# Performance work log

Measured on AMD Instinct MI355X. Metric: run time of the kernel, lower is better.

## Reference

```python
import jax, jax.numpy as jnp
import numpy as np

DENSE_SIZE = 2048
BATCH = 64
MAX_SPIKES = 1024


def setup_inputs() -> dict:
    key = jax.random.key(0)
    k_w, k_ids, k_ns = jax.random.split(key, 3)
    # weights ~ N(0, 2) as in tf.random_normal_initializer(0., 2., 42)
    W = jax.random.normal(k_w, (DENSE_SIZE, DENSE_SIZE), dtype=jnp.float32) * 2.0
    spike_ids = jax.random.randint(k_ids, (BATCH, MAX_SPIKES), 0, DENSE_SIZE, dtype=jnp.int32)
    num_spikes = jax.random.randint(k_ns, (BATCH,), 0, MAX_SPIKES, dtype=jnp.int32)
    return {"spike_ids": spike_ids, "num_spikes": num_spikes, "W": W}


def reference(spike_ids, num_spikes, W):
    # Dense-weight x binary-sparse-vector matmul:
    # out[b, j] = sum_{i < num_spikes[b]} W[j, spike_ids[b, i]]
    # i.e. gather active columns of W and sum them.
    mask = (jnp.arange(MAX_SPIKES)[None, :] < num_spikes[:, None]).astype(W.dtype)  # [B, S]
    cols = jnp.take(W.T, spike_ids, axis=0)  # [B, S, D] gathered columns (rows of W.T)
    out = jnp.einsum('bs,bsd->bd', mask, cols)  # [B, D]
    return out
```

## Files before the change

kernel.cpp:

```cpp
#include <hip/hip_runtime.h>

#define DENSE 2048
#define BATCH 64
#define MAXS  1024

typedef __attribute__((ext_vector_type(8))) __bf16 bf16x8;
typedef __attribute__((ext_vector_type(4))) float f32x4;


__global__ __launch_bounds__(256) void hist_kernel(const int* __restrict__ ids,
                                                   const int* __restrict__ ns,
                                                   __bf16* __restrict__ Cbf,
                                                   float* __restrict__ out) {
    __shared__ int cnt[DENSE];
    const int b = blockIdx.x;
    const int tid = threadIdx.x;
    #pragma unroll
    for (int k = tid; k < DENSE; k += 256) cnt[k] = 0;
    __syncthreads();
    const int n = ns[b];
    const int4 v = ((const int4*)(ids + b * MAXS))[tid];
    const int base = tid * 4;
    if (base + 0 < n) atomicAdd(&cnt[v.x], 1);
    if (base + 1 < n) atomicAdd(&cnt[v.y], 1);
    if (base + 2 < n) atomicAdd(&cnt[v.z], 1);
    if (base + 3 < n) atomicAdd(&cnt[v.w], 1);
    __syncthreads();
    const int mt = b >> 4;
    const int bl = b & 15;
    #pragma unroll
    for (int k = tid; k < DENSE; k += 256) {
        const int lane = bl | (((k >> 3) & 3) << 4);
        const size_t off = (size_t)(((k >> 5) * 4 + mt) * 64 + lane) * 8 + (k & 7);
        Cbf[off] = (__bf16)(float)cnt[k];
        out[(size_t)b * DENSE + k] = 0.0f;
    }
}

__global__ __launch_bounds__(256) void spmm_kernel(const float* __restrict__ W,
                                                   const __bf16* __restrict__ Cbf,
                                                   float* __restrict__ out) {
    const int tid  = threadIdx.x;
    const int lane = tid & 63;
    const int wv   = tid >> 6;
    const int j0   = blockIdx.x * 16;
    const int ks4  = blockIdx.y;

    const int ln = lane & 15;
    const int lq = lane >> 4;

    const int step0 = ks4 * 16 + wv * 4;
    const float* wrow = W + (size_t)(j0 + ln) * DENSE;

    f32x4 w0[4], w1[4];
    #pragma unroll
    for (int s = 0; s < 4; ++s) {
        const int kbase = (step0 + s) * 32 + lq * 8;
        w0[s] = *(const f32x4*)(wrow + kbase);
        w1[s] = *(const f32x4*)(wrow + kbase + 4);
    }
    bf16x8 afr[4][4];
    #pragma unroll
    for (int s = 0; s < 4; ++s) {
        #pragma unroll
        for (int mt = 0; mt < 4; ++mt) {
            afr[s][mt] = *(const bf16x8*)(Cbf + ((size_t)((step0 + s) * 4 + mt) * 64 + lane) * 8);
        }
    }

    bf16x8 wb[4];
    #pragma unroll
    for (int s = 0; s < 4; ++s) {
        #pragma unroll
        for (int i = 0; i < 4; ++i) {
            wb[s][i]     = (__bf16)w0[s][i];
            wb[s][i + 4] = (__bf16)w1[s][i];
        }
    }

    f32x4 acc[4];
    #pragma unroll
    for (int mt = 0; mt < 4; ++mt) acc[mt] = (f32x4)0.0f;
    #pragma unroll
    for (int s = 0; s < 4; ++s) {
        #pragma unroll
        for (int mt = 0; mt < 4; ++mt) {
            acc[mt] = __builtin_amdgcn_mfma_f32_16x16x32_bf16(afr[s][mt], wb[s], acc[mt], 0, 0, 0);
        }
    }

    __shared__ float P[4][4][4][64];
    #pragma unroll
    for (int mt = 0; mt < 4; ++mt) {
        #pragma unroll
        for (int r = 0; r < 4; ++r) {
            P[wv][mt][r][lane] = acc[mt][r];
        }
    }
    __syncthreads();

    const int jloc  = tid & 15;
    const int bpart = tid >> 4;
    const int lsrc  = ((bpart >> 2) << 4) | jloc;
    const int r     = bpart & 3;
    #pragma unroll
    for (int mt = 0; mt < 4; ++mt) {
        const float v = P[0][mt][r][lsrc] + P[1][mt][r][lsrc]
                      + P[2][mt][r][lsrc] + P[3][mt][r][lsrc];
        atomicAdd(&out[(size_t)(mt * 16 + bpart) * DENSE + j0 + jloc], v);
    }
}

extern "C" void kernel_launch(void* const* d_in, const int* in_sizes, int n_in,
                              void* d_out, int out_size, void* d_ws, size_t ws_size,
                              hipStream_t stream) {
    const int*   ids = (const int*)d_in[0];
    const int*   ns  = (const int*)d_in[1];
    const float* W   = (const float*)d_in[2];
    float*  out = (float*)d_out;
    __bf16* Cbf = (__bf16*)d_ws;

    hipLaunchKernelGGL(hist_kernel, dim3(BATCH), dim3(256), 0, stream, ids, ns, Cbf, out);
    hipLaunchKernelGGL(spmm_kernel, dim3(128, 4), dim3(256), 0, stream, W, Cbf, out);
}
```

Measured before the change: 71.39 us.

## Fuse histogram and SpMM into one cooperative kernel with grid sync

Merges the histogram and MFMA SpMM kernels into one cooperative launch of 512 blocks. The first 64 blocks build the per-batch count matrix and zero the output, and every block prefetches and converts its W tile before a grid-wide barrier. After the barrier the blocks read the counts and run the MFMA accumulation. This removes the second kernel launch and overlaps the W loads with the histogram work, at the cost of a grid sync and a cooperative launch that needs all blocks resident at once.

```diff
diff --git a/kernel.cpp b/kernel.cpp
--- a/kernel.cpp
+++ b/kernel.cpp
@@ -1,54 +1,32 @@
 #include <hip/hip_runtime.h>
+#include <hip/hip_cooperative_groups.h>
 
 #define DENSE 2048
 #define BATCH 64
 #define MAXS  1024
 
+namespace cg = cooperative_groups;
+
 typedef __attribute__((ext_vector_type(8))) __bf16 bf16x8;
 typedef __attribute__((ext_vector_type(4))) float f32x4;
 
 
-__global__ __launch_bounds__(256) void hist_kernel(const int* __restrict__ ids,
-                                                   const int* __restrict__ ns,
-                                                   __bf16* __restrict__ Cbf,
-                                                   float* __restrict__ out) {
-    __shared__ int cnt[DENSE];
-    const int b = blockIdx.x;
-    const int tid = threadIdx.x;
-    #pragma unroll
-    for (int k = tid; k < DENSE; k += 256) cnt[k] = 0;
-    __syncthreads();
-    const int n = ns[b];
-    const int4 v = ((const int4*)(ids + b * MAXS))[tid];
-    const int base = tid * 4;
-    if (base + 0 < n) atomicAdd(&cnt[v.x], 1);
-    if (base + 1 < n) atomicAdd(&cnt[v.y], 1);
-    if (base + 2 < n) atomicAdd(&cnt[v.z], 1);
-    if (base + 3 < n) atomicAdd(&cnt[v.w], 1);
-    __syncthreads();
-    const int mt = b >> 4;
-    const int bl = b & 15;
-    #pragma unroll
-    for (int k = tid; k < DENSE; k += 256) {
-        const int lane = bl | (((k >> 3) & 3) << 4);
-        const size_t off = (size_t)(((k >> 5) * 4 + mt) * 64 + lane) * 8 + (k & 7);
-        Cbf[off] = (__bf16)(float)cnt[k];
-        out[(size_t)b * DENSE + k] = 0.0f;
-    }
-}
+__global__ __launch_bounds__(256, 2) void fused_kernel(
+        const int* __restrict__ ids, const int* __restrict__ ns,
+        const float* __restrict__ W, __bf16* __restrict__ Cbf,
+        float* __restrict__ out) {
+    __shared__ int   cnt[DENSE];
+    __shared__ float P[4][4][4][64];
 
-__global__ __launch_bounds__(256) void spmm_kernel(const float* __restrict__ W,
-                                                   const __bf16* __restrict__ Cbf,
-                                                   float* __restrict__ out) {
     const int tid  = threadIdx.x;
+    const int bid  = blockIdx.x;
+    const int jt   = bid & 127;
+    const int ks4  = bid >> 7;
     const int lane = tid & 63;
     const int wv   = tid >> 6;
-    const int j0   = blockIdx.x * 16;
-    const int ks4  = blockIdx.y;
-
-    const int ln = lane & 15;
-    const int lq = lane >> 4;
-
+    const int ln   = lane & 15;
+    const int lq   = lane >> 4;
+    const int j0   = jt * 16;
     const int step0 = ks4 * 16 + wv * 4;
     const float* wrow = W + (size_t)(j0 + ln) * DENSE;
 
@@ -59,12 +37,28 @@
         w0[s] = *(const f32x4*)(wrow + kbase);
         w1[s] = *(const f32x4*)(wrow + kbase + 4);
     }
-    bf16x8 afr[4][4];
-    #pragma unroll
-    for (int s = 0; s < 4; ++s) {
+
+    if (bid < BATCH) {
+        const int b = bid;
         #pragma unroll
-        for (int mt = 0; mt < 4; ++mt) {
-            afr[s][mt] = *(const bf16x8*)(Cbf + ((size_t)((step0 + s) * 4 + mt) * 64 + lane) * 8);
+        for (int k = tid; k < DENSE; k += 256) cnt[k] = 0;
+        __syncthreads();
+        const int n = ns[b];
+        const int4 v = ((const int4*)(ids + b * MAXS))[tid];
+        const int base = tid * 4;
+        if (base + 0 < n) atomicAdd(&cnt[v.x], 1);
+        if (base + 1 < n) atomicAdd(&cnt[v.y], 1);
+        if (base + 2 < n) atomicAdd(&cnt[v.z], 1);
+        if (base + 3 < n) atomicAdd(&cnt[v.w], 1);
+        __syncthreads();
+        const int mt = b >> 4;
+        const int bl = b & 15;
+        #pragma unroll
+        for (int k = tid; k < DENSE; k += 256) {
+            const int l2 = bl | (((k >> 3) & 3) << 4);
+            const size_t off = (size_t)(((k >> 5) * 4 + mt) * 64 + l2) * 8 + (k & 7);
+            Cbf[off] = (__bf16)(float)cnt[k];
+            out[(size_t)b * DENSE + k] = 0.0f;
         }
     }
 
@@ -75,6 +69,17 @@
         for (int i = 0; i < 4; ++i) {
             wb[s][i]     = (__bf16)w0[s][i];
             wb[s][i + 4] = (__bf16)w1[s][i];
+        }
+    }
+
+    cg::this_grid().sync();
+
+    bf16x8 afr[4][4];
+    #pragma unroll
+    for (int s = 0; s < 4; ++s) {
+        #pragma unroll
+        for (int mt = 0; mt < 4; ++mt) {
+            afr[s][mt] = *(const bf16x8*)(Cbf + ((size_t)((step0 + s) * 4 + mt) * 64 + lane) * 8);
         }
     }
 
@@ -89,7 +94,6 @@
         }
     }
 
-    __shared__ float P[4][4][4][64];
     #pragma unroll
     for (int mt = 0; mt < 4; ++mt) {
         #pragma unroll
@@ -120,6 +124,6 @@
     float*  out = (float*)d_out;
     __bf16* Cbf = (__bf16*)d_ws;
 
-    hipLaunchKernelGGL(hist_kernel, dim3(BATCH), dim3(256), 0, stream, ids, ns, Cbf, out);
-    hipLaunchKernelGGL(spmm_kernel, dim3(128, 4), dim3(256), 0, stream, W, Cbf, out);
+    void* args[] = {(void*)&ids, (void*)&ns, (void*)&W, (void*)&Cbf, (void*)&out};
+    hipLaunchCooperativeKernel(fused_kernel, dim3(512), dim3(256), args, 0, stream);
 }
```

After: 155.6 us. 118% more time.

## Reduce full K in one block, drop output zeroing and global atomics

Applied to the files above, without the earlier changes.

The spmm kernel now uses 1024-thread blocks, one per 16-column tile. All 16 waves cover the whole K dimension and reduce through shared memory, so each output is written directly instead of with atomicAdd. This removes the need for the histogram kernel to zero the output, and that kernel now writes its bf16 counts with vectorized int4 loads and 16-byte stores. The grid shrinks from 512 to 128 blocks, which may leave CUs underused and adds a larger 16-way shared-memory reduction.

```diff
diff --git a/kernel.cpp b/kernel.cpp
--- a/kernel.cpp
+++ b/kernel.cpp
@@ -10,13 +10,12 @@
 
 __global__ __launch_bounds__(256) void hist_kernel(const int* __restrict__ ids,
                                                    const int* __restrict__ ns,
-                                                   __bf16* __restrict__ Cbf,
-                                                   float* __restrict__ out) {
+                                                   __bf16* __restrict__ Cbf) {
     __shared__ int cnt[DENSE];
     const int b = blockIdx.x;
     const int tid = threadIdx.x;
-    #pragma unroll
-    for (int k = tid; k < DENSE; k += 256) cnt[k] = 0;
+    ((int4*)cnt)[tid]       = int4{0, 0, 0, 0};
+    ((int4*)cnt)[tid + 256] = int4{0, 0, 0, 0};
     __syncthreads();
     const int n = ns[b];
     const int4 v = ((const int4*)(ids + b * MAXS))[tid];
@@ -28,28 +27,30 @@
     __syncthreads();
     const int mt = b >> 4;
     const int bl = b & 15;
-    #pragma unroll
-    for (int k = tid; k < DENSE; k += 256) {
-        const int lane = bl | (((k >> 3) & 3) << 4);
-        const size_t off = (size_t)(((k >> 5) * 4 + mt) * 64 + lane) * 8 + (k & 7);
-        Cbf[off] = (__bf16)(float)cnt[k];
-        out[(size_t)b * DENSE + k] = 0.0f;
-    }
+    const int l2 = bl | ((tid & 3) << 4);
+    const size_t off = ((size_t)((tid >> 2) * 4 + mt) * 64 + l2) * 8;
+    const int4 c0 = ((const int4*)cnt)[tid * 2];
+    const int4 c1 = ((const int4*)cnt)[tid * 2 + 1];
+    bf16x8 o;
+    o[0] = (__bf16)(float)c0.x;  o[1] = (__bf16)(float)c0.y;
+    o[2] = (__bf16)(float)c0.z;  o[3] = (__bf16)(float)c0.w;
+    o[4] = (__bf16)(float)c1.x;  o[5] = (__bf16)(float)c1.y;
+    o[6] = (__bf16)(float)c1.z;  o[7] = (__bf16)(float)c1.w;
+    *(bf16x8*)(Cbf + off) = o;
 }
 
-__global__ __launch_bounds__(256) void spmm_kernel(const float* __restrict__ W,
-                                                   const __bf16* __restrict__ Cbf,
-                                                   float* __restrict__ out) {
+__global__ __launch_bounds__(1024, 1) void spmm_kernel(const float* __restrict__ W,
+                                                       const __bf16* __restrict__ Cbf,
+                                                       float* __restrict__ out) {
+    __shared__ float P[16][16][64];
+
     const int tid  = threadIdx.x;
     const int lane = tid & 63;
     const int wv   = tid >> 6;
     const int j0   = blockIdx.x * 16;
-    const int ks4  = blockIdx.y;
-
-    const int ln = lane & 15;
-    const int lq = lane >> 4;
-
-    const int step0 = ks4 * 16 + wv * 4;
+    const int ln   = lane & 15;
+    const int lq   = lane >> 4;
+    const int step0 = wv * 4;
     const float* wrow = W + (size_t)(j0 + ln) * DENSE;
 
     f32x4 w0[4], w1[4];
@@ -68,47 +69,42 @@
         }
     }
 
-    bf16x8 wb[4];
-    #pragma unroll
-    for (int s = 0; s < 4; ++s) {
-        #pragma unroll
-        for (int i = 0; i < 4; ++i) {
-            wb[s][i]     = (__bf16)w0[s][i];
-            wb[s][i + 4] = (__bf16)w1[s][i];
-        }
-    }
-
     f32x4 acc[4];
     #pragma unroll
     for (int mt = 0; mt < 4; ++mt) acc[mt] = (f32x4)0.0f;
     #pragma unroll
     for (int s = 0; s < 4; ++s) {
+        bf16x8 wb;
+        #pragma unroll
+        for (int i = 0; i < 4; ++i) {
+            wb[i]     = (__bf16)w0[s][i];
+            wb[i + 4] = (__bf16)w1[s][i];
+        }
         #pragma unroll
         for (int mt = 0; mt < 4; ++mt) {
-            acc[mt] = __builtin_amdgcn_mfma_f32_16x16x32_bf16(afr[s][mt], wb[s], acc[mt], 0, 0, 0);
+            acc[mt] = __builtin_amdgcn_mfma_f32_16x16x32_bf16(afr[s][mt], wb, acc[mt], 0, 0, 0);
         }
     }
 
-    __shared__ float P[4][4][4][64];
     #pragma unroll
     for (int mt = 0; mt < 4; ++mt) {
         #pragma unroll
         for (int r = 0; r < 4; ++r) {
-            P[wv][mt][r][lane] = acc[mt][r];
+            P[wv][mt * 4 + r][lane] = acc[mt][r];
         }
     }
     __syncthreads();
 
     const int jloc  = tid & 15;
-    const int bpart = tid >> 4;
+    const int brow  = tid >> 4;
+    const int mt    = brow >> 4;
+    const int bpart = brow & 15;
     const int lsrc  = ((bpart >> 2) << 4) | jloc;
     const int r     = bpart & 3;
+    float v = 0.0f;
     #pragma unroll
-    for (int mt = 0; mt < 4; ++mt) {
-        const float v = P[0][mt][r][lsrc] + P[1][mt][r][lsrc]
-                      + P[2][mt][r][lsrc] + P[3][mt][r][lsrc];
-        atomicAdd(&out[(size_t)(mt * 16 + bpart) * DENSE + j0 + jloc], v);
-    }
+    for (int w = 0; w < 16; ++w) v += P[w][mt * 4 + r][lsrc];
+    out[(size_t)brow * DENSE + j0 + jloc] = v;
 }
 
 extern "C" void kernel_launch(void* const* d_in, const int* in_sizes, int n_in,
@@ -120,6 +116,6 @@
     float*  out = (float*)d_out;
     __bf16* Cbf = (__bf16*)d_ws;
 
-    hipLaunchKernelGGL(hist_kernel, dim3(BATCH), dim3(256), 0, stream, ids, ns, Cbf, out);
-    hipLaunchKernelGGL(spmm_kernel, dim3(128, 4), dim3(256), 0, stream, W, Cbf, out);
+    hipLaunchKernelGGL(hist_kernel, dim3(BATCH), dim3(256), 0, stream, ids, ns, Cbf);
+    hipLaunchKernelGGL(spmm_kernel, dim3(DENSE / 16), dim3(1024), 0, stream, W, Cbf, out);
 }
```

After: 73.83 us. +3.4%, slower.
